# Optimization experiments

Hardware: AMD Instinct MI355X
Metric: run time of the kernel (lower is better)

The kernel has to match this reference:

```python
import jax, jax.numpy as jnp
import numpy as np

N = 50000      # nodes
E = 800000     # edges (avg degree 16)
F_IN = 32
H = 64         # hidden_features
E_DIM = 16     # edge_dim
C_OUT = 40
L = 2          # num_layers
G = 64         # graphs in batch
BN_EPS = 1e-5
GEN_EPS = 1e-7  # PyG GENConv message eps


def setup_inputs() -> dict:
    key = jax.random.key(0)
    ks = jax.random.split(key, 12)
    s = 0.05
    inp = {}
    inp["x"] = jax.random.normal(ks[0], (N, F_IN), jnp.float32)
    inp["edge_index"] = jax.random.randint(ks[1], (2, E), 0, N)
    inp["edge_attr"] = jax.random.normal(ks[2], (E, E_DIM), jnp.float32)
    inp["batch"] = jnp.sort(jax.random.randint(ks[3], (N,), 0, G))
    # input linear
    inp["lin_in_w"] = jax.random.normal(ks[4], (F_IN, H), jnp.float32) * s
    inp["lin_in_b"] = jnp.zeros((H,), jnp.float32)
    # per-layer DeepGCNLayer norm (BatchNorm affine)
    inp["norm_gamma"] = jnp.ones((L, H), jnp.float32)
    inp["norm_beta"] = jnp.zeros((L, H), jnp.float32)
    # per-layer GENConv params
    inp["edge_w"] = jax.random.normal(ks[5], (L, E_DIM, H), jnp.float32) * s
    inp["edge_b"] = jnp.zeros((L, H), jnp.float32)
    inp["t"] = jnp.ones((L,), jnp.float32)  # learned softmax temperature
    inp["mlp_w1"] = jax.random.normal(ks[6], (L, H, 2 * H), jnp.float32) * s
    inp["mlp_b1"] = jnp.zeros((L, 2 * H), jnp.float32)
    inp["mlp_gamma"] = jnp.ones((L, 2 * H), jnp.float32)
    inp["mlp_beta"] = jnp.zeros((L, 2 * H), jnp.float32)
    inp["mlp_w2"] = jax.random.normal(ks[7], (L, 2 * H, H), jnp.float32) * s
    inp["mlp_b2"] = jnp.zeros((L, H), jnp.float32)
    # output linear
    inp["lin_out_w"] = jax.random.normal(ks[8], (H, C_OUT), jnp.float32) * s
    inp["lin_out_b"] = jnp.zeros((C_OUT,), jnp.float32)
    return inp


def _batch_norm(x, gamma, beta):
    mu = jnp.mean(x, axis=0)
    var = jnp.var(x, axis=0)
    return (x - mu) * jax.lax.rsqrt(var + BN_EPS) * gamma + beta


def _gen_conv(x, src, dst, e_emb, t, w1, b1, g1, be1, w2, b2):
    # message: relu(x_j + edge_emb) + eps   -> [E, H]
    m = jax.nn.relu(x[src] + e_emb) + GEN_EPS
    # softmax aggregation over destination neighborhoods with temperature t
    logits = m * t
    seg_max = jax.ops.segment_max(logits, dst, num_segments=N)      # [N, H]
    ex = jnp.exp(logits - seg_max[dst])                              # [E, H]
    denom = jax.ops.segment_sum(ex, dst, num_segments=N)            # [N, H]
    agg = jax.ops.segment_sum(ex * m, dst, num_segments=N) / (denom + 1e-16)
    # root add, then GENConv MLP: Linear(H,2H) -> BN -> ReLU -> Linear(2H,H)
    out = agg + x
    h = out @ w1 + b1
    h = jax.nn.relu(_batch_norm(h, g1, be1))
    return h @ w2 + b2


def reference(x, edge_index, edge_attr, batch, lin_in_w, lin_in_b,
              norm_gamma, norm_beta, edge_w, edge_b, t,
              mlp_w1, mlp_b1, mlp_gamma, mlp_beta, mlp_w2, mlp_b2,
              lin_out_w, lin_out_b):
    src, dst = edge_index[0], edge_index[1]
    h = x @ lin_in_w + lin_in_b                                      # [N, H]
    for l in range(L):
        # DeepGCNLayer res+ : norm -> act -> (dropout p=0) -> conv, residual add
        z = jax.nn.relu(_batch_norm(h, norm_gamma[l], norm_beta[l]))
        e_emb = edge_attr @ edge_w[l] + edge_b[l]                    # [E, H]
        c = _gen_conv(z, src, dst, e_emb, t[l], mlp_w1[l], mlp_b1[l],
                      mlp_gamma[l], mlp_beta[l], mlp_w2[l], mlp_b2[l])
        h = h + c
    # global mean pool per graph
    sums = jax.ops.segment_sum(h, batch, num_segments=G)             # [G, H]
    counts = jax.ops.segment_sum(jnp.ones((N, 1), h.dtype), batch, num_segments=G)
    pooled = sums / jnp.maximum(counts, 1.0)
    out = jax.nn.relu(pooled) @ lin_out_w + lin_out_b                # [G, C_OUT]
    return out
```

## Files before the change

kernel.cpp:

```cpp
#include <hip/hip_runtime.h>

#define N_NODES 50000
#define N_EDGES 800000
#define F_INP   32
#define HDIM    64
#define EDIM    16
#define COUT    40
#define NGRAPH  64
#define LDS_STRIDE 18

typedef float v2f __attribute__((ext_vector_type(2)));

__global__ void hist_kernel(const int* __restrict__ dst, int* __restrict__ cnt, int E) {
    int e = blockIdx.x * 256 + threadIdx.x;
    if (e < E) atomicAdd(&cnt[dst[e]], 1);
}

__global__ void scan_part_kernel(const int* __restrict__ cnt, int* __restrict__ bsum, int n) {
    __shared__ int red[256];
    int tid = threadIdx.x;
    int idx = blockIdx.x * 256 + tid;
    red[tid] = (idx < n) ? cnt[idx] : 0;
    __syncthreads();
    for (int off = 128; off > 0; off >>= 1) {
        if (tid < off) red[tid] += red[tid + off];
        __syncthreads();
    }
    if (tid == 0) bsum[blockIdx.x] = red[0];
}

__global__ void scan_top_kernel(int* __restrict__ bsum, int nb) {
    __shared__ int tmp[256];
    int tid = threadIdx.x;
    int v = (tid < nb) ? bsum[tid] : 0;
    tmp[tid] = v;
    __syncthreads();
    for (int off = 1; off < 256; off <<= 1) {
        int x = (tid >= off) ? tmp[tid - off] : 0;
        __syncthreads();
        tmp[tid] += x;
        __syncthreads();
    }
    if (tid < nb) bsum[tid] = tmp[tid] - v;
}

__global__ void scan_apply_kernel(const int* __restrict__ cnt, const int* __restrict__ bsum,
                                  int* __restrict__ offsets, int* __restrict__ cursor, int n) {
    __shared__ int tmp[256];
    int tid = threadIdx.x;
    int idx = blockIdx.x * 256 + tid;
    int v = (idx < n) ? cnt[idx] : 0;
    tmp[tid] = v;
    __syncthreads();
    for (int off = 1; off < 256; off <<= 1) {
        int x = (tid >= off) ? tmp[tid - off] : 0;
        __syncthreads();
        tmp[tid] += x;
        __syncthreads();
    }
    int excl = tmp[tid] - v + bsum[blockIdx.x];
    if (idx < n) { offsets[idx] = excl; cursor[idx] = excl; }
    if (idx == n - 1) offsets[n] = excl + v;
}

__global__ void scatter_kernel(const int* __restrict__ dst, const int* __restrict__ src,
                               int* __restrict__ cursor, int4* __restrict__ edge4, int E) {
    int e = blockIdx.x * 256 + threadIdx.x;
    if (e < E) {
        int d = dst[e];
        int p = atomicAdd(&cursor[d], 1);
        edge4[p] = make_int4(d, src[e], e, 0);
    }
}

__global__ void gstart_kernel(const int* __restrict__ batch, int* __restrict__ gstart,
                              int N, int G) {
    int n = blockIdx.x * 256 + threadIdx.x;
    if (n >= N) return;
    int g  = batch[n];
    int gp = (n == 0) ? -1 : batch[n - 1];
    for (int gg = gp + 1; gg <= g; gg++) gstart[gg] = n;
    if (n == N - 1) {
        for (int gg = g + 1; gg <= G; gg++) gstart[gg] = N;
    }
}

__global__ void lin_in_kernel(const float* __restrict__ x, const float* __restrict__ W,
                              const float* __restrict__ b, float* __restrict__ h, int N) {
    int tid = threadIdx.x;
    int c = tid & 63;
    float w[F_INP];
#pragma unroll
    for (int k = 0; k < F_INP; k++) w[k] = W[k * HDIM + c];
    int node = blockIdx.x * 4 + (tid >> 6);
    if (node >= N) return;
    const float4* xr = (const float4*)(x + (size_t)node * F_INP);
    float acc = b[c];
#pragma unroll
    for (int k4 = 0; k4 < F_INP / 4; k4++) {
        float4 xv = xr[k4];
        acc += xv.x * w[k4 * 4 + 0] + xv.y * w[k4 * 4 + 1]
             + xv.z * w[k4 * 4 + 2] + xv.w * w[k4 * 4 + 3];
    }
    h[(size_t)node * HDIM + c] = acc;
}

template <int C>
__global__ void bn_stats_kernel(const float* __restrict__ x, float* __restrict__ stats, int N) {
    const int RPB = 256 / C;
    int tid = threadIdx.x;
    int c = tid % C;
    int row0 = blockIdx.x * RPB + tid / C;
    int stride = gridDim.x * RPB;
    float s = 0.f, ss = 0.f;
    for (int r = row0; r < N; r += stride) {
        float v = x[(size_t)r * C + c];
        s += v; ss += v * v;
    }
    __shared__ float ls[256], lss[256];
    ls[tid] = s; lss[tid] = ss;
    __syncthreads();
    if (tid < C) {
        for (int k = 1; k < RPB; k++) { s += ls[tid + k * C]; ss += lss[tid + k * C]; }
        atomicAdd(&stats[c], s);
        atomicAdd(&stats[C + c], ss);
    }
}

__global__ __launch_bounds__(256) void edge_agg_kernel(
        const float* __restrict__ h, const float* __restrict__ ea,
        const int4* __restrict__ edge4,
        const float* __restrict__ We, const float* __restrict__ be,
        const float* __restrict__ tptr, const float* __restrict__ stats,
        const float* __restrict__ gamma, const float* __restrict__ beta,
        float* __restrict__ num, float* __restrict__ den) {
    __shared__ float sA[4 * 64 * LDS_STRIDE];
    int tid = threadIdx.x;
    int c  = tid & 63;
    int wv = tid >> 6;
    float inv = 1.0f / (float)N_NODES;
    float mu  = stats[c] * inv;
    float var = stats[HDIM + c] * inv - mu * mu;
    float sc  = rsqrtf(var + 1e-5f) * gamma[c];
    float sb  = beta[c] - mu * sc;
    v2f w2[8];
#pragma unroll
    for (int k = 0; k < 8; k++) {
        w2[k].x = We[(2 * k) * HDIM + c];
        w2[k].y = We[(2 * k + 1) * HDIM + c];
    }
    float bc = be[c];
    float tl2 = (*tptr) * 1.4426950408889634f;

    int p = (blockIdx.x * 4 + wv) * 64 + c;
    int4 pk = edge4[p];
    int d_own = pk.x;
    int s_own = pk.y;
    int e     = pk.z;
    float* myrow = &sA[(wv * 64 + c) * LDS_STRIDE];
    {
        const float4* ar = (const float4*)(ea + (size_t)e * EDIM);
        float4 a0 = ar[0], a1 = ar[1], a2 = ar[2], a3 = ar[3];
        myrow[0]=a0.x;  myrow[1]=a0.y;  myrow[2]=a0.z;  myrow[3]=a0.w;
        myrow[4]=a1.x;  myrow[5]=a1.y;  myrow[6]=a1.z;  myrow[7]=a1.w;
        myrow[8]=a2.x;  myrow[9]=a2.y;  myrow[10]=a2.z; myrow[11]=a2.w;
        myrow[12]=a3.x; myrow[13]=a3.y; myrow[14]=a3.z; myrow[15]=a3.w;
    }
    int dprev = __shfl_up(d_own, 1);
    unsigned long long bmask = __ballot(c > 0 && d_own != dprev);
    __syncthreads();

    const float* wrow = &sA[(size_t)wv * 64 * LDS_STRIDE];
    float nacc = 0.f, dacc = 0.f;
    int cur_d = __builtin_amdgcn_readlane(d_own, 0);
#pragma unroll 1
    for (int jj = 0; jj < 64; jj += 8) {
        float hv[8];
#pragma unroll
        for (int u = 0; u < 8; u++) {
            int su = __builtin_amdgcn_readlane(s_own, jj + u);
            hv[u] = h[(size_t)su * HDIM + c];
        }
#pragma unroll
        for (int u = 0; u < 8; u++) {
            if (bmask & (1ull << (jj + u))) {
                atomicAdd(&num[(size_t)cur_d * HDIM + c], nacc);
                atomicAdd(&den[(size_t)cur_d * HDIM + c], dacc);
                nacc = 0.f; dacc = 0.f;
                cur_d = __builtin_amdgcn_readlane(d_own, jj + u);
            }
            const v2f* arow = (const v2f*)&wrow[(jj + u) * LDS_STRIDE];
            v2f acc2 = {bc, 0.f};
#pragma unroll
            for (int k2 = 0; k2 < 8; k2++)
                acc2 += arow[k2] * w2[k2];
            float acc = acc2.x + acc2.y;
            float zv = fmaxf(hv[u] * sc + sb, 0.f);
            float m  = fmaxf(zv + acc, 0.f) + 1e-7f;
            float ex = exp2f(m * tl2);
            dacc += ex;
            nacc += ex * m;
        }
    }
    atomicAdd(&num[(size_t)cur_d * HDIM + c], nacc);
    atomicAdd(&den[(size_t)cur_d * HDIM + c], dacc);
}

__global__ __launch_bounds__(256) void mlp1_kernel(
        float* __restrict__ num, float* __restrict__ den,
        const float* __restrict__ h, const float* __restrict__ stats,
        const float* __restrict__ gamma, const float* __restrict__ beta,
        const float* __restrict__ W1, const float* __restrict__ b1,
        float* __restrict__ h1, int N) {
    __shared__ float sW[HDIM * 128];
    __shared__ float srow[32 * 65];
    int tid = threadIdx.x;
    for (int i = tid; i < HDIM * 128; i += 256) sW[i] = W1[i];
    int base = blockIdx.x * 32;
    {
        int cc = tid & 63;
        float inv = 1.0f / (float)N_NODES;
        float mu  = stats[cc] * inv;
        float var = stats[HDIM + cc] * inv - mu * mu;
        float rs  = rsqrtf(var + 1e-5f);
        float ga  = gamma[cc], bb = beta[cc];
        for (int i = tid; i < 32 * HDIM; i += 256) {
            int r = i >> 6;
            int node = base + r;
            float v = 0.f;
            if (node < N) {
                size_t idx = (size_t)node * HDIM + cc;
                float hv = h[idx];
                float z  = fmaxf((hv - mu) * rs * ga + bb, 0.f);
                float nu = num[idx], de = den[idx];
                num[idx] = 0.f; den[idx] = 0.f;
                v = nu / (de + 1e-16f) + z;
            }
            srow[r * 65 + cc] = v;
        }
    }
    __syncthreads();
    int tx = tid & 31;
    int ty = tid >> 5;
    float acc[4][4];
    float b0 = b1[4 * tx], bb1 = b1[4 * tx + 1], b2v = b1[4 * tx + 2], b3 = b1[4 * tx + 3];
#pragma unroll
    for (int j = 0; j < 4; j++) { acc[j][0] = b0; acc[j][1] = bb1; acc[j][2] = b2v; acc[j][3] = b3; }
#pragma unroll 8
    for (int k = 0; k < HDIM; k++) {
        float4 wv = *(const float4*)&sW[k * 128 + 4 * tx];
        float r0 = srow[(ty * 4 + 0) * 65 + k];
        float r1 = srow[(ty * 4 + 1) * 65 + k];
        float r2 = srow[(ty * 4 + 2) * 65 + k];
        float r3 = srow[(ty * 4 + 3) * 65 + k];
        acc[0][0] += r0 * wv.x; acc[0][1] += r0 * wv.y; acc[0][2] += r0 * wv.z; acc[0][3] += r0 * wv.w;
        acc[1][0] += r1 * wv.x; acc[1][1] += r1 * wv.y; acc[1][2] += r1 * wv.z; acc[1][3] += r1 * wv.w;
        acc[2][0] += r2 * wv.x; acc[2][1] += r2 * wv.y; acc[2][2] += r2 * wv.z; acc[2][3] += r2 * wv.w;
        acc[3][0] += r3 * wv.x; acc[3][1] += r3 * wv.y; acc[3][2] += r3 * wv.z; acc[3][3] += r3 * wv.w;
    }
#pragma unroll
    for (int j = 0; j < 4; j++) {
        int node = base + ty * 4 + j;
        if (node < N)
            *(float4*)&h1[(size_t)node * 128 + 4 * tx] =
                make_float4(acc[j][0], acc[j][1], acc[j][2], acc[j][3]);
    }
}

__global__ __launch_bounds__(256) void mlp2_kernel(
        const float* __restrict__ h1, const float* __restrict__ stats,
        const float* __restrict__ mg, const float* __restrict__ mb,
        const float* __restrict__ W2, const float* __restrict__ b2,
        float* __restrict__ h, int N) {
    __shared__ float sW[128 * HDIM];
    __shared__ float sact[32 * 129];
    __shared__ float sbn[4 * 128];
    int tid = threadIdx.x;
    for (int i = tid; i < 128 * HDIM; i += 256) sW[i] = W2[i];
    if (tid < 128) {
        float inv = 1.0f / (float)N;
        float mu  = stats[tid] * inv;
        float var = stats[128 + tid] * inv - mu * mu;
        sbn[tid]       = mu;
        sbn[128 + tid] = rsqrtf(var + 1e-5f);
        sbn[256 + tid] = mg[tid];
        sbn[384 + tid] = mb[tid];
    }
    __syncthreads();
    int base = blockIdx.x * 32;
    for (int i = tid; i < 32 * 128; i += 256) {
        int r = i >> 7, o = i & 127;
        int node = base + r;
        float v = 0.f;
        if (node < N) {
            v = h1[(size_t)node * 128 + o];
            v = fmaxf((v - sbn[o]) * sbn[128 + o] * sbn[256 + o] + sbn[384 + o], 0.f);
        }
        sact[r * 129 + o] = v;
    }
    __syncthreads();
    int tx = tid & 15;
    int ty = tid >> 4;
    float acc[2][4];
    float b0 = b2[4 * tx], bb1 = b2[4 * tx + 1], b2v = b2[4 * tx + 2], b3 = b2[4 * tx + 3];
    acc[0][0] = b0; acc[0][1] = bb1; acc[0][2] = b2v; acc[0][3] = b3;
    acc[1][0] = b0; acc[1][1] = bb1; acc[1][2] = b2v; acc[1][3] = b3;
#pragma unroll 8
    for (int k = 0; k < 128; k++) {
        float4 wv = *(const float4*)&sW[k * HDIM + 4 * tx];
        float r0 = sact[(ty * 2 + 0) * 129 + k];
        float r1 = sact[(ty * 2 + 1) * 129 + k];
        acc[0][0] += r0 * wv.x; acc[0][1] += r0 * wv.y; acc[0][2] += r0 * wv.z; acc[0][3] += r0 * wv.w;
        acc[1][0] += r1 * wv.x; acc[1][1] += r1 * wv.y; acc[1][2] += r1 * wv.z; acc[1][3] += r1 * wv.w;
    }
#pragma unroll
    for (int j = 0; j < 2; j++) {
        int node = base + ty * 2 + j;
        if (node < N) {
            float4* p = (float4*)&h[(size_t)node * HDIM + 4 * tx];
            float4 old = *p;
            *p = make_float4(old.x + acc[j][0], old.y + acc[j][1],
                             old.z + acc[j][2], old.w + acc[j][3]);
        }
    }
}

__global__ void pool_out_kernel(const float* __restrict__ h, const int* __restrict__ gstart,
                                const float* __restrict__ Wo, const float* __restrict__ bo,
                                float* __restrict__ out, int N) {
    __shared__ float sp[HDIM];
    __shared__ float red[256];
    __shared__ float sW[HDIM * COUT];
    int g = blockIdx.x;
    int tid = threadIdx.x;
    for (int i = tid; i < HDIM * COUT; i += 256) sW[i] = Wo[i];
    int beg = gstart[g], end = gstart[g + 1];
    int c = tid & 63, r0 = tid >> 6;
    float s = 0.f;
    for (int r = beg + r0; r < end; r += 4) s += h[(size_t)r * HDIM + c];
    red[tid] = s;
    __syncthreads();
    if (tid < HDIM) {
        s = red[tid] + red[tid + 64] + red[tid + 128] + red[tid + 192];
        float cnt = (float)(end - beg);
        float pooled = s / fmaxf(cnt, 1.0f);
        sp[tid] = fmaxf(pooled, 0.0f);
    }
    __syncthreads();
    if (tid < COUT) {
        float acc = bo[tid];
#pragma unroll
        for (int k = 0; k < HDIM; k++) acc += sp[k] * sW[k * COUT + tid];
        out[g * COUT + tid] = acc;
    }
}

extern "C" void kernel_launch(void* const* d_in, const int* in_sizes, int n_in,
                              void* d_out, int out_size, void* d_ws, size_t ws_size,
                              hipStream_t stream) {
    (void)in_sizes; (void)n_in; (void)out_size; (void)ws_size;
    const float* x          = (const float*)d_in[0];
    const int*   eidx       = (const int*)  d_in[1];
    const float* eattr      = (const float*)d_in[2];
    const int*   batch      = (const int*)  d_in[3];
    const float* lin_in_w   = (const float*)d_in[4];
    const float* lin_in_b   = (const float*)d_in[5];
    const float* norm_gamma = (const float*)d_in[6];
    const float* norm_beta  = (const float*)d_in[7];
    const float* edge_w     = (const float*)d_in[8];
    const float* edge_b     = (const float*)d_in[9];
    const float* tparam     = (const float*)d_in[10];
    const float* mlp_w1     = (const float*)d_in[11];
    const float* mlp_b1     = (const float*)d_in[12];
    const float* mlp_gamma  = (const float*)d_in[13];
    const float* mlp_beta   = (const float*)d_in[14];
    const float* mlp_w2     = (const float*)d_in[15];
    const float* mlp_b2     = (const float*)d_in[16];
    const float* lin_out_w  = (const float*)d_in[17];
    const float* lin_out_b  = (const float*)d_in[18];
    float* out = (float*)d_out;

    const int* src = eidx;
    const int* dst = eidx + N_EDGES;

    char* ws = (char*)d_ws;
    size_t off = 0;
    auto alloc = [&](size_t bytes) -> char* {
        char* p = ws + off;
        off = (off + bytes + 255) & ~(size_t)255;
        return p;
    };
    int*   cnt     = (int*)  alloc((size_t)N_NODES * 4);
    float* statsA0 = (float*)alloc(128 * 4);
    float* statsB0 = (float*)alloc(256 * 4);
    float* statsA1 = (float*)alloc(128 * 4);
    float* statsB1 = (float*)alloc(256 * 4);
    size_t zero_bytes = off;
    int*   bsum    = (int*)  alloc(256 * 4);
    int*   offsets = (int*)  alloc((size_t)(N_NODES + 1) * 4);
    int*   cursor  = (int*)  alloc((size_t)N_NODES * 4);
    int4*  edge4   = (int4*) alloc((size_t)N_EDGES * 16);
    int*   gstart  = (int*)  alloc((size_t)(NGRAPH + 1) * 4);
    float* h       = (float*)alloc((size_t)N_NODES * HDIM * 4);
    float* num     = (float*)alloc((size_t)N_NODES * HDIM * 4);
    float* den     = (float*)alloc((size_t)N_NODES * HDIM * 4);
    float* h1      = (float*)alloc((size_t)N_NODES * 2 * HDIM * 4);

    hipMemsetAsync(d_ws, 0, zero_bytes, stream);
    hipMemsetAsync(num, 0, (size_t)N_NODES * HDIM * 4 * 2, stream);

    const int NB = (N_NODES + 255) / 256;
    hist_kernel      <<<(N_EDGES + 255) / 256, 256, 0, stream>>>(dst, cnt, N_EDGES);
    scan_part_kernel <<<NB, 256, 0, stream>>>(cnt, bsum, N_NODES);
    scan_top_kernel  <<<1, 256, 0, stream>>>(bsum, NB);
    scan_apply_kernel<<<NB, 256, 0, stream>>>(cnt, bsum, offsets, cursor, N_NODES);
    scatter_kernel   <<<(N_EDGES + 255) / 256, 256, 0, stream>>>(dst, src, cursor, edge4, N_EDGES);
    gstart_kernel    <<<NB, 256, 0, stream>>>(batch, gstart, N_NODES, NGRAPH);
    lin_in_kernel    <<<(N_NODES + 3) / 4, 256, 0, stream>>>(x, lin_in_w, lin_in_b, h, N_NODES);

    const int AGG_BLOCKS = N_EDGES / 256;

    float* statsA[2] = { statsA0, statsA1 };
    float* statsB[2] = { statsB0, statsB1 };
    for (int l = 0; l < 2; l++) {
        bn_stats_kernel<64><<<256, 256, 0, stream>>>(h, statsA[l], N_NODES);
        edge_agg_kernel<<<AGG_BLOCKS, 256, 0, stream>>>(
            h, eattr, edge4,
            edge_w + (size_t)l * EDIM * HDIM, edge_b + l * HDIM,
            tparam + l, statsA[l], norm_gamma + l * HDIM, norm_beta + l * HDIM,
            num, den);
        mlp1_kernel<<<(N_NODES + 31) / 32, 256, 0, stream>>>(
            num, den, h, statsA[l], norm_gamma + l * HDIM, norm_beta + l * HDIM,
            mlp_w1 + (size_t)l * HDIM * 2 * HDIM, mlp_b1 + l * 2 * HDIM, h1, N_NODES);
        bn_stats_kernel<128><<<256, 256, 0, stream>>>(h1, statsB[l], N_NODES);
        mlp2_kernel<<<(N_NODES + 31) / 32, 256, 0, stream>>>(
            h1, statsB[l], mlp_gamma + l * 2 * HDIM, mlp_beta + l * 2 * HDIM,
            mlp_w2 + (size_t)l * 2 * HDIM * HDIM, mlp_b2 + l * HDIM, h, N_NODES);
    }
    pool_out_kernel<<<NGRAPH, 256, 0, stream>>>(h, gstart, lin_out_w, lin_out_b, out, N_NODES);
}
```

Before: 631.8 us.

## Drop CSR edge sort and aggregate with per-edge atomics in original order

Removes the histogram/scan/scatter kernels that sorted edges by destination, and processes edges in their input order. Each edge now atomically adds its numerator and denominator directly into the destination row instead of merging runs of same-destination edges in registers. This removes several preprocessing launches and makes edge_attr reads coalesced. In exchange it multiplies the number of random global float atomics by roughly the average degree.

```diff
diff --git a/kernel.cpp b/kernel.cpp
--- a/kernel.cpp
+++ b/kernel.cpp
@@ -10,68 +10,6 @@
 #define LDS_STRIDE 18
 
 typedef float v2f __attribute__((ext_vector_type(2)));
-
-__global__ void hist_kernel(const int* __restrict__ dst, int* __restrict__ cnt, int E) {
-    int e = blockIdx.x * 256 + threadIdx.x;
-    if (e < E) atomicAdd(&cnt[dst[e]], 1);
-}
-
-__global__ void scan_part_kernel(const int* __restrict__ cnt, int* __restrict__ bsum, int n) {
-    __shared__ int red[256];
-    int tid = threadIdx.x;
-    int idx = blockIdx.x * 256 + tid;
-    red[tid] = (idx < n) ? cnt[idx] : 0;
-    __syncthreads();
-    for (int off = 128; off > 0; off >>= 1) {
-        if (tid < off) red[tid] += red[tid + off];
-        __syncthreads();
-    }
-    if (tid == 0) bsum[blockIdx.x] = red[0];
-}
-
-__global__ void scan_top_kernel(int* __restrict__ bsum, int nb) {
-    __shared__ int tmp[256];
-    int tid = threadIdx.x;
-    int v = (tid < nb) ? bsum[tid] : 0;
-    tmp[tid] = v;
-    __syncthreads();
-    for (int off = 1; off < 256; off <<= 1) {
-        int x = (tid >= off) ? tmp[tid - off] : 0;
-        __syncthreads();
-        tmp[tid] += x;
-        __syncthreads();
-    }
-    if (tid < nb) bsum[tid] = tmp[tid] - v;
-}
-
-__global__ void scan_apply_kernel(const int* __restrict__ cnt, const int* __restrict__ bsum,
-                                  int* __restrict__ offsets, int* __restrict__ cursor, int n) {
-    __shared__ int tmp[256];
-    int tid = threadIdx.x;
-    int idx = blockIdx.x * 256 + tid;
-    int v = (idx < n) ? cnt[idx] : 0;
-    tmp[tid] = v;
-    __syncthreads();
-    for (int off = 1; off < 256; off <<= 1) {
-        int x = (tid >= off) ? tmp[tid - off] : 0;
-        __syncthreads();
-        tmp[tid] += x;
-        __syncthreads();
-    }
-    int excl = tmp[tid] - v + bsum[blockIdx.x];
-    if (idx < n) { offsets[idx] = excl; cursor[idx] = excl; }
-    if (idx == n - 1) offsets[n] = excl + v;
-}
-
-__global__ void scatter_kernel(const int* __restrict__ dst, const int* __restrict__ src,
-                               int* __restrict__ cursor, int4* __restrict__ edge4, int E) {
-    int e = blockIdx.x * 256 + threadIdx.x;
-    if (e < E) {
-        int d = dst[e];
-        int p = atomicAdd(&cursor[d], 1);
-        edge4[p] = make_int4(d, src[e], e, 0);
-    }
-}
 
 __global__ void gstart_kernel(const int* __restrict__ batch, int* __restrict__ gstart,
                               int N, int G) {
@@ -128,8 +66,8 @@
 }
 
 __global__ __launch_bounds__(256) void edge_agg_kernel(
-        const float* __restrict__ h, const float* __restrict__ ea,
-        const int4* __restrict__ edge4,
+        const float* __restrict__ h, const int* __restrict__ src,
+        const int* __restrict__ dst, const float* __restrict__ ea,
         const float* __restrict__ We, const float* __restrict__ be,
         const float* __restrict__ tptr, const float* __restrict__ stats,
         const float* __restrict__ gamma, const float* __restrict__ beta,
@@ -153,26 +91,20 @@
     float tl2 = (*tptr) * 1.4426950408889634f;
 
     int p = (blockIdx.x * 4 + wv) * 64 + c;
-    int4 pk = edge4[p];
-    int d_own = pk.x;
-    int s_own = pk.y;
-    int e     = pk.z;
+    int d_own = dst[p];
+    int s_own = src[p];
     float* myrow = &sA[(wv * 64 + c) * LDS_STRIDE];
     {
-        const float4* ar = (const float4*)(ea + (size_t)e * EDIM);
+        const float4* ar = (const float4*)(ea + (size_t)p * EDIM);
         float4 a0 = ar[0], a1 = ar[1], a2 = ar[2], a3 = ar[3];
         myrow[0]=a0.x;  myrow[1]=a0.y;  myrow[2]=a0.z;  myrow[3]=a0.w;
         myrow[4]=a1.x;  myrow[5]=a1.y;  myrow[6]=a1.z;  myrow[7]=a1.w;
         myrow[8]=a2.x;  myrow[9]=a2.y;  myrow[10]=a2.z; myrow[11]=a2.w;
         myrow[12]=a3.x; myrow[13]=a3.y; myrow[14]=a3.z; myrow[15]=a3.w;
     }
-    int dprev = __shfl_up(d_own, 1);
-    unsigned long long bmask = __ballot(c > 0 && d_own != dprev);
     __syncthreads();
 
     const float* wrow = &sA[(size_t)wv * 64 * LDS_STRIDE];
-    float nacc = 0.f, dacc = 0.f;
-    int cur_d = __builtin_amdgcn_readlane(d_own, 0);
 #pragma unroll 1
     for (int jj = 0; jj < 64; jj += 8) {
         float hv[8];
@@ -183,12 +115,7 @@
         }
 #pragma unroll
         for (int u = 0; u < 8; u++) {
-            if (bmask & (1ull << (jj + u))) {
-                atomicAdd(&num[(size_t)cur_d * HDIM + c], nacc);
-                atomicAdd(&den[(size_t)cur_d * HDIM + c], dacc);
-                nacc = 0.f; dacc = 0.f;
-                cur_d = __builtin_amdgcn_readlane(d_own, jj + u);
-            }
+            int du = __builtin_amdgcn_readlane(d_own, jj + u);
             const v2f* arow = (const v2f*)&wrow[(jj + u) * LDS_STRIDE];
             v2f acc2 = {bc, 0.f};
 #pragma unroll
@@ -198,12 +125,11 @@
             float zv = fmaxf(hv[u] * sc + sb, 0.f);
             float m  = fmaxf(zv + acc, 0.f) + 1e-7f;
             float ex = exp2f(m * tl2);
-            dacc += ex;
-            nacc += ex * m;
-        }
-    }
-    atomicAdd(&num[(size_t)cur_d * HDIM + c], nacc);
-    atomicAdd(&den[(size_t)cur_d * HDIM + c], dacc);
+            size_t idx = (size_t)du * HDIM + c;
+            atomicAdd(&num[idx], ex * m);
+            atomicAdd(&den[idx], ex);
+        }
+    }
 }
 
 __global__ __launch_bounds__(256) void mlp1_kernel(
@@ -390,16 +316,11 @@
         off = (off + bytes + 255) & ~(size_t)255;
         return p;
     };
-    int*   cnt     = (int*)  alloc((size_t)N_NODES * 4);
     float* statsA0 = (float*)alloc(128 * 4);
     float* statsB0 = (float*)alloc(256 * 4);
     float* statsA1 = (float*)alloc(128 * 4);
     float* statsB1 = (float*)alloc(256 * 4);
     size_t zero_bytes = off;
-    int*   bsum    = (int*)  alloc(256 * 4);
-    int*   offsets = (int*)  alloc((size_t)(N_NODES + 1) * 4);
-    int*   cursor  = (int*)  alloc((size_t)N_NODES * 4);
-    int4*  edge4   = (int4*) alloc((size_t)N_EDGES * 16);
     int*   gstart  = (int*)  alloc((size_t)(NGRAPH + 1) * 4);
     float* h       = (float*)alloc((size_t)N_NODES * HDIM * 4);
     float* num     = (float*)alloc((size_t)N_NODES * HDIM * 4);
@@ -410,13 +331,8 @@
     hipMemsetAsync(num, 0, (size_t)N_NODES * HDIM * 4 * 2, stream);
 
     const int NB = (N_NODES + 255) / 256;
-    hist_kernel      <<<(N_EDGES + 255) / 256, 256, 0, stream>>>(dst, cnt, N_EDGES);
-    scan_part_kernel <<<NB, 256, 0, stream>>>(cnt, bsum, N_NODES);
-    scan_top_kernel  <<<1, 256, 0, stream>>>(bsum, NB);
-    scan_apply_kernel<<<NB, 256, 0, stream>>>(cnt, bsum, offsets, cursor, N_NODES);
-    scatter_kernel   <<<(N_EDGES + 255) / 256, 256, 0, stream>>>(dst, src, cursor, edge4, N_EDGES);
-    gstart_kernel    <<<NB, 256, 0, stream>>>(batch, gstart, N_NODES, NGRAPH);
-    lin_in_kernel    <<<(N_NODES + 3) / 4, 256, 0, stream>>>(x, lin_in_w, lin_in_b, h, N_NODES);
+    gstart_kernel <<<NB, 256, 0, stream>>>(batch, gstart, N_NODES, NGRAPH);
+    lin_in_kernel <<<(N_NODES + 3) / 4, 256, 0, stream>>>(x, lin_in_w, lin_in_b, h, N_NODES);
 
     const int AGG_BLOCKS = N_EDGES / 256;
 
@@ -425,7 +341,7 @@
     for (int l = 0; l < 2; l++) {
         bn_stats_kernel<64><<<256, 256, 0, stream>>>(h, statsA[l], N_NODES);
         edge_agg_kernel<<<AGG_BLOCKS, 256, 0, stream>>>(
-            h, eattr, edge4,
+            h, src, dst, eattr,
             edge_w + (size_t)l * EDIM * HDIM, edge_b + l * HDIM,
             tparam + l, statsA[l], norm_gamma + l * HDIM, norm_beta + l * HDIM,
             num, den);
```

Result: slower. 1.066 ms (+68.8%).
